# Optimization experiments

Hardware: AMD Instinct MI355X
Metric: run time of the kernel (lower is better)

The kernel has to match this reference:

```python
import jax, jax.numpy as jnp
import numpy as np

N_HEAD = 25

def setup_inputs() -> dict:
    key = jax.random.key(0)
    k1, k2, k3 = jax.random.split(key, 3)
    B, T, C = 2, 2048, 1600
    x = jax.random.normal(k1, (B, T, C), dtype=jnp.float32)
    w_qkv = jax.random.normal(k2, (C, 3 * C), dtype=jnp.float32) * (1.0 / np.sqrt(C))
    b_qkv = jnp.zeros((3 * C,), dtype=jnp.float32)
    w_out = jax.random.normal(k3, (C, C), dtype=jnp.float32) * (1.0 / np.sqrt(C))
    b_out = jnp.zeros((C,), dtype=jnp.float32)
    return {"x": x, "w_qkv": w_qkv, "b_qkv": b_qkv, "w_out": w_out, "b_out": b_out}

def reference(x, w_qkv, b_qkv, w_out, b_out):
    B, T, C = x.shape
    H = N_HEAD
    D = C // H  # head_dim = 64
    qkv = jnp.einsum('btc,cd->btd', x, w_qkv) + b_qkv  # [B,T,3C]
    q, k, v = jnp.split(qkv, 3, axis=-1)
    # [B,T,C] -> [B,H,T,D]
    q = q.reshape(B, T, H, D).transpose(0, 2, 1, 3)
    k = k.reshape(B, T, H, D).transpose(0, 2, 1, 3)
    v = v.reshape(B, T, H, D).transpose(0, 2, 1, 3)
    scale = 1.0 / jnp.sqrt(jnp.float32(D))
    scores = jnp.einsum('bhqd,bhkd->bhqk', q, k) * scale  # [B,H,T,T]
    causal = jnp.tril(jnp.ones((T, T), dtype=bool))
    scores = jnp.where(causal, scores, jnp.float32(-1e10))
    attn = jax.nn.softmax(scores, axis=-1)
    out = jnp.einsum('bhqk,bhkd->bhqd', attn, v)  # [B,H,T,D]
    out = out.transpose(0, 2, 1, 3).reshape(B, T, C)
    return jnp.einsum('btc,cd->btd', out, w_out) + b_out
```

## Files before the change

kernel.cpp:

```cpp
#include <hip/hip_runtime.h>
#include <cstdint>
#include <cstddef>

typedef unsigned short u16;
typedef __attribute__((ext_vector_type(8))) short bhalf8;
typedef __attribute__((ext_vector_type(4))) float fx4;
typedef __attribute__((ext_vector_type(4))) unsigned short u16x4;

#define T_SEQ 2048
#define NHEAD 25
#define QKV_LD 4864

static __device__ __forceinline__ u16 f2bf(float f) {
  union { float f; uint32_t u; } v; v.f = f;
  uint32_t r = (v.u + 0x7FFFu + ((v.u >> 16) & 1u)) >> 16;
  return (u16)r;
}

static __device__ __forceinline__ fx4 mfma16(bhalf8 a, bhalf8 b, fx4 c) {
  return __builtin_amdgcn_mfma_f32_16x16x32_bf16(a, b, c, 0, 0, 0);
}

static __device__ __forceinline__ void async16(const void* g, void* l) {
  __builtin_amdgcn_global_load_lds(
      (__attribute__((address_space(1))) unsigned int*)(void*)g,
      (__attribute__((address_space(3))) unsigned int*)l, 16, 0, 0);
}

__global__ void cvt_bf16_kernel(const float* __restrict__ in, u16* __restrict__ out, int n4) {
  int i = blockIdx.x * 256 + threadIdx.x;
  if (i >= n4) return;
  float4 v = ((const float4*)in)[i];
  u16x4 o;
  o.x = f2bf(v.x); o.y = f2bf(v.y); o.z = f2bf(v.z); o.w = f2bf(v.w);
  ((u16x4*)out)[i] = o;
}

__global__ void transp_cvt_kernel(const float* __restrict__ in, u16* __restrict__ out,
                                  int R, int C) {
  __shared__ float tile[32][33];
  int bx = blockIdx.x * 32, by = blockIdx.y * 32;
  int tx = threadIdx.x, ty = threadIdx.y;
  #pragma unroll
  for (int i = 0; i < 32; i += 8)
    tile[ty + i][tx] = in[(size_t)(by + ty + i) * C + bx + tx];
  __syncthreads();
  #pragma unroll
  for (int i = 0; i < 32; i += 8)
    out[(size_t)(bx + ty + i) * R + by + tx] = f2bf(tile[tx][ty + i]);
}

template<int BN, bool OUTF32>
__global__ __launch_bounds__(256)
void gemm_bt_kernel(const u16* __restrict__ A, const u16* __restrict__ BT,
                    const float* __restrict__ bias, void* __restrict__ C,
                    int K, int ldc, int Nreal) {
  constexpr int BM = 128, BK = 32;
  constexpr int NF = BN / 32;
  constexpr int APASS = (BM * BK) / (256 * 8);
  constexpr int BPASS = (BN * BK) / (256 * 8);
  __shared__ __align__(16) u16 Al[BM * BK];
  __shared__ __align__(16) u16 Bl[BN * BK];
  const int t = threadIdx.x;
  const int w = t >> 6, l = t & 63, lr = l & 15, lg = l >> 4;
  const int wm = w >> 1, wn = w & 1;

  const int nwg = gridDim.x * gridDim.y;
  const int id = blockIdx.y * gridDim.x + blockIdx.x;
  const int qq = nwg >> 3;
  const int swz = (id & 7) * qq + (id >> 3);
  const int bx = swz % gridDim.x, by = swz / gridDim.x;

  const int m0 = by * BM, n0 = bx * BN;

  fx4 acc[4][NF] = {};

  for (int k0 = 0; k0 < K; k0 += BK) {
    #pragma unroll
    for (int p = 0; p < APASS; ++p) {
      int c = t + p * 256;
      async16(A + (size_t)(m0 + (c >> 2)) * K + k0 + (c & 3) * 8, Al + c * 8);
    }
    #pragma unroll
    for (int p = 0; p < BPASS; ++p) {
      int c = t + p * 256;
      async16(BT + (size_t)(n0 + (c >> 2)) * K + k0 + (c & 3) * 8, Bl + c * 8);
    }
    __syncthreads();
    bhalf8 af[4], bfr[NF];
    #pragma unroll
    for (int m = 0; m < 4; ++m)
      af[m] = *(const bhalf8*)(Al + (wm * 64 + m * 16 + lr) * BK + lg * 8);
    #pragma unroll
    for (int n = 0; n < NF; ++n)
      bfr[n] = *(const bhalf8*)(Bl + (wn * (BN / 2) + n * 16 + lr) * BK + lg * 8);
    #pragma unroll
    for (int m = 0; m < 4; ++m)
      #pragma unroll
      for (int n = 0; n < NF; ++n)
        acc[m][n] = mfma16(af[m], bfr[n], acc[m][n]);
    __syncthreads();
  }

  #pragma unroll
  for (int m = 0; m < 4; ++m)
  #pragma unroll
  for (int n = 0; n < NF; ++n)
  #pragma unroll
  for (int r = 0; r < 4; ++r) {
    int gr = m0 + wm * 64 + m * 16 + lg * 4 + r;
    int gc = n0 + wn * (BN / 2) + n * 16 + lr;
    float bv = (gc < Nreal) ? bias[gc] : 0.0f;
    float v = acc[m][n][r] + bv;
    if constexpr (OUTF32) ((float*)C)[(size_t)gr * ldc + gc] = v;
    else                  ((u16*)C)[(size_t)gr * ldc + gc] = f2bf(v);
  }
}

#define KSWZ(row, slot) (((row) << 6) + ((((slot)) ^ ((row) & 7)) << 3))

__global__ __launch_bounds__(512, 4)
void attn_kernel(const u16* __restrict__ qkv, u16* __restrict__ out) {
  const int qblk = (gridDim.x - 1) - blockIdx.x;
  const int bh = blockIdx.y;
  const int b = bh / NHEAD, h = bh % NHEAD;
  const int t = threadIdx.x, w = t >> 6, l = t & 63;
  const int lr = l & 15, lg = l >> 4;

  __shared__ __align__(16) u16 Kl[2][64 * 64];
  __shared__ __align__(16) u16 Vt[2][64 * 64];
  __shared__ __align__(16) u16 Pl[8][16][72];

  const int q0 = qblk * 128;
  const int qw = q0 + w * 16;
  const int nkb = 2 * qblk + 2;

  const size_t qoff = ((size_t)(b * T_SEQ + qw + lr)) * QKV_LD + h * 64;
  bhalf8 qf0 = *(const bhalf8*)(qkv + qoff + lg * 8);
  bhalf8 qf1 = *(const bhalf8*)(qkv + qoff + 32 + lg * 8);

  constexpr float KSC = 0.125f * 1.44269504089f;

  fx4 oacc[4] = {};
  float m_run[4], mk[4], thr[4], l_acc[4];
  #pragma unroll
  for (int r = 0; r < 4; ++r) {
    m_run[r] = -3.0e38f; mk[r] = -3.0e38f; thr[r] = -3.0e38f; l_acc[r] = 0.0f;
  }

  const int krow = t >> 3;
  const int kslot = (t & 7) ^ (krow & 7);
  const int vrow = t >> 3;
  const int vcol = (t & 7) * 8;
  const size_t kvrow_base = (size_t)(b * T_SEQ) * QKV_LD + 1600 + h * 64;

  int4 vpre;
  {
    const size_t ks = kvrow_base + (size_t)krow * QKV_LD + kslot * 8;
    async16(qkv + ks, Kl[0] + t * 8);
    vpre = *(const int4*)(qkv + kvrow_base + (size_t)vrow * QKV_LD + 1600 + vcol);
  }

  for (int kb = 0; kb < nkb; ++kb) {
    const int bsel = kb & 1;
    const int kv0 = kb * 64;
    u16* Klb = Kl[bsel];
    u16* Vtb = Vt[bsel];

    asm volatile("s_waitcnt vmcnt(0)" ::: "memory");
    {
      union { int4 v; u16 u[8]; } vv; vv.v = vpre;
      #pragma unroll
      for (int i = 0; i < 8; ++i) {
        int row = vcol + i;
        Vtb[(row << 6) + (((vrow >> 3) ^ (row & 7)) << 3) + (vrow & 7)] = vv.u[i];
      }
    }
    __syncthreads();

    if (kb + 1 < nkb) {
      const size_t rb = kvrow_base + (size_t)(kv0 + 64 + krow) * QKV_LD;
      async16(qkv + rb + kslot * 8, Kl[bsel ^ 1] + t * 8);
      vpre = *(const int4*)(qkv + kvrow_base + (size_t)(kv0 + 64 + vrow) * QKV_LD + 1600 + vcol);
    }

    const bool active = (kv0 <= qw + 15);
    if (active) {
      float sv[4][4];
      #pragma unroll
      for (int n = 0; n < 4; ++n) {
        bhalf8 k0f = *(const bhalf8*)(Klb + KSWZ(n * 16 + lr, lg));
        bhalf8 k1f = *(const bhalf8*)(Klb + KSWZ(n * 16 + lr, 4 + lg));
        fx4 s = {0.f, 0.f, 0.f, 0.f};
        s = mfma16(qf0, k0f, s);
        s = mfma16(qf1, k1f, s);
        #pragma unroll
        for (int r = 0; r < 4; ++r) sv[n][r] = s[r];
      }
      if (kv0 + 63 > qw) {
        #pragma unroll
        for (int n = 0; n < 4; ++n)
          #pragma unroll
          for (int r = 0; r < 4; ++r)
            if (kv0 + n * 16 + lr > qw + lg * 4 + r) sv[n][r] = -1e30f;
      }
      float pm[4];
      bool ok = true;
      #pragma unroll
      for (int r = 0; r < 4; ++r) {
        pm[r] = fmaxf(fmaxf(sv[0][r], sv[1][r]), fmaxf(sv[2][r], sv[3][r]));
        ok = ok && (pm[r] <= thr[r]);
      }
      if (!__all(ok)) {
        #pragma unroll
        for (int r = 0; r < 4; ++r) {
          float mx = pm[r] * 0.125f;
          mx = fmaxf(mx, __shfl_xor(mx, 1));
          mx = fmaxf(mx, __shfl_xor(mx, 2));
          mx = fmaxf(mx, __shfl_xor(mx, 4));
          mx = fmaxf(mx, __shfl_xor(mx, 8));
          float mN = fmaxf(m_run[r], mx);
          float scl = __expf(m_run[r] - mN);
          m_run[r] = mN;
          mk[r] = mN * 1.44269504089f;
          thr[r] = 8.0f * mN + 64.0f;
          l_acc[r] *= scl;
          oacc[0][r] *= scl; oacc[1][r] *= scl; oacc[2][r] *= scl; oacc[3][r] *= scl;
        }
      }
      #pragma unroll
      for (int n = 0; n < 4; ++n)
        #pragma unroll
        for (int r = 0; r < 4; ++r) {
          float p = exp2f(fmaf(sv[n][r], KSC, -mk[r]));
          l_acc[r] += p;
          Pl[w][lg * 4 + r][n * 16 + lr] = f2bf(p);
        }
      asm volatile("s_waitcnt lgkmcnt(0)" ::: "memory");
      __builtin_amdgcn_sched_barrier(0);
      #pragma unroll
      for (int s = 0; s < 2; ++s) {
        bhalf8 pa = *(const bhalf8*)&Pl[w][lr][s * 32 + lg * 8];
        #pragma unroll
        for (int n = 0; n < 4; ++n) {
          bhalf8 vbf = *(const bhalf8*)(Vtb + KSWZ(n * 16 + lr, s * 4 + lg));
          oacc[n] = mfma16(pa, vbf, oacc[n]);
        }
      }
    }
  }

  #pragma unroll
  for (int r = 0; r < 4; ++r) {
    float rs = l_acc[r];
    rs += __shfl_xor(rs, 1);
    rs += __shfl_xor(rs, 2);
    rs += __shfl_xor(rs, 4);
    rs += __shfl_xor(rs, 8);
    l_acc[r] = rs;
  }
  const size_t obase = ((size_t)(b * T_SEQ + qw + lg * 4)) * 1600 + h * 64;
  #pragma unroll
  for (int n = 0; n < 4; ++n)
    #pragma unroll
    for (int r = 0; r < 4; ++r) {
      float v = oacc[n][r] / l_acc[r];
      out[obase + (size_t)r * 1600 + n * 16 + lr] = f2bf(v);
    }
}

extern "C" void kernel_launch(void* const* d_in, const int* in_sizes, int n_in,
                              void* d_out, int out_size, void* d_ws, size_t ws_size,
                              hipStream_t stream) {
  const float* x     = (const float*)d_in[0];
  const float* w_qkv = (const float*)d_in[1];
  const float* b_qkv = (const float*)d_in[2];
  const float* w_out = (const float*)d_in[3];
  const float* b_out = (const float*)d_in[4];
  float* out = (float*)d_out;

  constexpr size_t NTOK = 4096;
  char* ws = (char*)d_ws;
  size_t off = 0;
  u16* xb    = (u16*)(ws + off); off += NTOK * 1600 * 2;
  u16* wqkvT = (u16*)(ws + off); off += (size_t)QKV_LD * 1600 * 2;
  u16* woutT = (u16*)(ws + off); off += (size_t)1600 * 1600 * 2;
  u16* qkvb  = (u16*)(ws + off); off += NTOK * QKV_LD * 2;
  u16* attnb = (u16*)(ws + off); off += NTOK * 1600 * 2;
  (void)ws_size; (void)in_sizes; (void)n_in; (void)out_size;

  cvt_bf16_kernel<<<dim3((unsigned)(NTOK * 1600 / 4 / 256)), dim3(256), 0, stream>>>(
      x, xb, (int)(NTOK * 1600 / 4));
  transp_cvt_kernel<<<dim3(4800 / 32, 1600 / 32), dim3(32, 8), 0, stream>>>(
      w_qkv, wqkvT, 1600, 4800);
  transp_cvt_kernel<<<dim3(1600 / 32, 1600 / 32), dim3(32, 8), 0, stream>>>(
      w_out, woutT, 1600, 1600);
  gemm_bt_kernel<128, false><<<dim3(QKV_LD / 128, NTOK / 128), dim3(256), 0, stream>>>(
      xb, wqkvT, b_qkv, qkvb, 1600, QKV_LD, 4800);
  attn_kernel<<<dim3(T_SEQ / 128, 2 * NHEAD), dim3(512), 0, stream>>>(qkvb, attnb);
  gemm_bt_kernel<64, true><<<dim3(1600 / 64, NTOK / 128), dim3(256), 0, stream>>>(
      attnb, woutT, b_out, out, 1600, 1600, 1600);
}
```

Baseline: 437.4 us.

## Give each attention wave two query tiles and widen output GEMM tile

The attention kernel drops to 4 waves per block, and each wave now handles 32 query rows as two 16-row groups. Each K/V fragment read from LDS is reused across two MFMAs, which halves LDS traffic per unit of compute, at the cost of more registers and less occupancy. MFMA sections are wrapped in s_setprio. The output projection switches to a 128-wide N tile with a padded weight buffer (1664 columns) and a column guard on the store. The padded weight rows beyond 1600 are never written by the transpose, so they hold whatever was in the workspace, but their results are masked out.

```diff
diff --git a/kernel.cpp b/kernel.cpp
--- a/kernel.cpp
+++ b/kernel.cpp
@@ -10,6 +10,7 @@
 #define T_SEQ 2048
 #define NHEAD 25
 #define QKV_LD 4864
+#define WOUT_LD 1664
 
 static __device__ __forceinline__ u16 f2bf(float f) {
   union { float f; uint32_t u; } v; v.f = f;
@@ -112,14 +113,17 @@
     int gc = n0 + wn * (BN / 2) + n * 16 + lr;
     float bv = (gc < Nreal) ? bias[gc] : 0.0f;
     float v = acc[m][n][r] + bv;
-    if constexpr (OUTF32) ((float*)C)[(size_t)gr * ldc + gc] = v;
-    else                  ((u16*)C)[(size_t)gr * ldc + gc] = f2bf(v);
+    if constexpr (OUTF32) {
+      if (gc < Nreal) ((float*)C)[(size_t)gr * ldc + gc] = v;
+    } else {
+      ((u16*)C)[(size_t)gr * ldc + gc] = f2bf(v);
+    }
   }
 }
 
 #define KSWZ(row, slot) (((row) << 6) + ((((slot)) ^ ((row) & 7)) << 3))
 
-__global__ __launch_bounds__(512, 4)
+__global__ __launch_bounds__(256, 3)
 void attn_kernel(const u16* __restrict__ qkv, u16* __restrict__ out) {
   const int qblk = (gridDim.x - 1) - blockIdx.x;
   const int bh = blockIdx.y;
@@ -129,36 +133,42 @@
 
   __shared__ __align__(16) u16 Kl[2][64 * 64];
   __shared__ __align__(16) u16 Vt[2][64 * 64];
-  __shared__ __align__(16) u16 Pl[8][16][72];
+  __shared__ __align__(16) u16 Pl[4][32][72];
 
   const int q0 = qblk * 128;
-  const int qw = q0 + w * 16;
+  const int qw = q0 + w * 32;
   const int nkb = 2 * qblk + 2;
 
-  const size_t qoff = ((size_t)(b * T_SEQ + qw + lr)) * QKV_LD + h * 64;
-  bhalf8 qf0 = *(const bhalf8*)(qkv + qoff + lg * 8);
-  bhalf8 qf1 = *(const bhalf8*)(qkv + qoff + 32 + lg * 8);
+  bhalf8 qf[2][2];
+  #pragma unroll
+  for (int g = 0; g < 2; ++g) {
+    const size_t qoff = ((size_t)(b * T_SEQ + qw + g * 16 + lr)) * QKV_LD + h * 64;
+    qf[g][0] = *(const bhalf8*)(qkv + qoff + lg * 8);
+    qf[g][1] = *(const bhalf8*)(qkv + qoff + 32 + lg * 8);
+  }
 
   constexpr float KSC = 0.125f * 1.44269504089f;
 
-  fx4 oacc[4] = {};
-  float m_run[4], mk[4], thr[4], l_acc[4];
-  #pragma unroll
-  for (int r = 0; r < 4; ++r) {
-    m_run[r] = -3.0e38f; mk[r] = -3.0e38f; thr[r] = -3.0e38f; l_acc[r] = 0.0f;
-  }
-
-  const int krow = t >> 3;
-  const int kslot = (t & 7) ^ (krow & 7);
-  const int vrow = t >> 3;
-  const int vcol = (t & 7) * 8;
+  fx4 oacc[2][4] = {};
+  float m_run[2][4], mk[2][4], thr[2][4], l_acc[2][4];
+  #pragma unroll
+  for (int g = 0; g < 2; ++g)
+    #pragma unroll
+    for (int r = 0; r < 4; ++r) {
+      m_run[g][r] = -3.0e38f; mk[g][r] = -3.0e38f; thr[g][r] = -3.0e38f; l_acc[g][r] = 0.0f;
+    }
+
   const size_t kvrow_base = (size_t)(b * T_SEQ) * QKV_LD + 1600 + h * 64;
 
-  int4 vpre;
-  {
-    const size_t ks = kvrow_base + (size_t)krow * QKV_LD + kslot * 8;
-    async16(qkv + ks, Kl[0] + t * 8);
-    vpre = *(const int4*)(qkv + kvrow_base + (size_t)vrow * QKV_LD + 1600 + vcol);
+  int4 vpre[2];
+  #pragma unroll
+  for (int p = 0; p < 2; ++p) {
+    const int c = t + p * 256;
+    const int kr = c >> 3;
+    const int ks = (c & 7) ^ (kr & 7);
+    const size_t rb = kvrow_base + (size_t)kr * QKV_LD;
+    async16(qkv + rb + ks * 8, Kl[0] + c * 8);
+    vpre[p] = *(const int4*)(qkv + rb + 1600 + (c & 7) * 8);
   }
 
   for (int kb = 0; kb < nkb; ++kb) {
@@ -168,105 +178,136 @@
     u16* Vtb = Vt[bsel];
 
     asm volatile("s_waitcnt vmcnt(0)" ::: "memory");
-    {
-      union { int4 v; u16 u[8]; } vv; vv.v = vpre;
+    #pragma unroll
+    for (int p = 0; p < 2; ++p) {
+      const int c = t + p * 256;
+      const int vr = c >> 3;
+      const int vc = (c & 7) * 8;
+      union { int4 v; u16 u[8]; } vv; vv.v = vpre[p];
       #pragma unroll
       for (int i = 0; i < 8; ++i) {
-        int row = vcol + i;
-        Vtb[(row << 6) + (((vrow >> 3) ^ (row & 7)) << 3) + (vrow & 7)] = vv.u[i];
+        int row = vc + i;
+        Vtb[(row << 6) + (((vr >> 3) ^ (row & 7)) << 3) + (vr & 7)] = vv.u[i];
       }
     }
     __syncthreads();
 
     if (kb + 1 < nkb) {
-      const size_t rb = kvrow_base + (size_t)(kv0 + 64 + krow) * QKV_LD;
-      async16(qkv + rb + kslot * 8, Kl[bsel ^ 1] + t * 8);
-      vpre = *(const int4*)(qkv + kvrow_base + (size_t)(kv0 + 64 + vrow) * QKV_LD + 1600 + vcol);
-    }
-
-    const bool active = (kv0 <= qw + 15);
+      #pragma unroll
+      for (int p = 0; p < 2; ++p) {
+        const int c = t + p * 256;
+        const int kr = c >> 3;
+        const int ks = (c & 7) ^ (kr & 7);
+        const size_t rb = kvrow_base + (size_t)(kv0 + 64 + kr) * QKV_LD;
+        async16(qkv + rb + ks * 8, Kl[bsel ^ 1] + c * 8);
+        vpre[p] = *(const int4*)(qkv + rb + 1600 + (c & 7) * 8);
+      }
+    }
+
+    const bool active = (kv0 <= qw + 31);
     if (active) {
-      float sv[4][4];
+      float sv[2][4][4];
+      __builtin_amdgcn_s_setprio(1);
       #pragma unroll
       for (int n = 0; n < 4; ++n) {
         bhalf8 k0f = *(const bhalf8*)(Klb + KSWZ(n * 16 + lr, lg));
         bhalf8 k1f = *(const bhalf8*)(Klb + KSWZ(n * 16 + lr, 4 + lg));
-        fx4 s = {0.f, 0.f, 0.f, 0.f};
-        s = mfma16(qf0, k0f, s);
-        s = mfma16(qf1, k1f, s);
-        #pragma unroll
-        for (int r = 0; r < 4; ++r) sv[n][r] = s[r];
-      }
+        #pragma unroll
+        for (int g = 0; g < 2; ++g) {
+          fx4 s = {0.f, 0.f, 0.f, 0.f};
+          s = mfma16(qf[g][0], k0f, s);
+          s = mfma16(qf[g][1], k1f, s);
+          #pragma unroll
+          for (int r = 0; r < 4; ++r) sv[g][n][r] = s[r];
+        }
+      }
+      __builtin_amdgcn_s_setprio(0);
       if (kv0 + 63 > qw) {
+        #pragma unroll
+        for (int g = 0; g < 2; ++g)
+          #pragma unroll
+          for (int n = 0; n < 4; ++n)
+            #pragma unroll
+            for (int r = 0; r < 4; ++r)
+              if (kv0 + n * 16 + lr > qw + g * 16 + lg * 4 + r) sv[g][n][r] = -1e30f;
+      }
+      float pm[2][4];
+      bool ok = true;
+      #pragma unroll
+      for (int g = 0; g < 2; ++g)
+        #pragma unroll
+        for (int r = 0; r < 4; ++r) {
+          pm[g][r] = fmaxf(fmaxf(sv[g][0][r], sv[g][1][r]), fmaxf(sv[g][2][r], sv[g][3][r]));
+          ok = ok && (pm[g][r] <= thr[g][r]);
+        }
+      if (!__all(ok)) {
+        #pragma unroll
+        for (int g = 0; g < 2; ++g)
+          #pragma unroll
+          for (int r = 0; r < 4; ++r) {
+            float mx = pm[g][r] * 0.125f;
+            mx = fmaxf(mx, __shfl_xor(mx, 1));
+            mx = fmaxf(mx, __shfl_xor(mx, 2));
+            mx = fmaxf(mx, __shfl_xor(mx, 4));
+            mx = fmaxf(mx, __shfl_xor(mx, 8));
+            float mN = fmaxf(m_run[g][r], mx);
+            float scl = __expf(m_run[g][r] - mN);
+            m_run[g][r] = mN;
+            mk[g][r] = mN * 1.44269504089f;
+            thr[g][r] = 8.0f * mN + 64.0f;
+            l_acc[g][r] *= scl;
+            oacc[g][0][r] *= scl; oacc[g][1][r] *= scl;
+            oacc[g][2][r] *= scl; oacc[g][3][r] *= scl;
+          }
+      }
+      #pragma unroll
+      for (int g = 0; g < 2; ++g)
         #pragma unroll
         for (int n = 0; n < 4; ++n)
           #pragma unroll
-          for (int r = 0; r < 4; ++r)
-            if (kv0 + n * 16 + lr > qw + lg * 4 + r) sv[n][r] = -1e30f;
-      }
-      float pm[4];
-      bool ok = true;
-      #pragma unroll
-      for (int r = 0; r < 4; ++r) {
-        pm[r] = fmaxf(fmaxf(sv[0][r], sv[1][r]), fmaxf(sv[2][r], sv[3][r]));
-        ok = ok && (pm[r] <= thr[r]);
-      }
-      if (!__all(ok)) {
-        #pragma unroll
-        for (int r = 0; r < 4; ++r) {
-          float mx = pm[r] * 0.125f;
-          mx = fmaxf(mx, __shfl_xor(mx, 1));
-          mx = fmaxf(mx, __shfl_xor(mx, 2));
-          mx = fmaxf(mx, __shfl_xor(mx, 4));
-          mx = fmaxf(mx, __shfl_xor(mx, 8));
-          float mN = fmaxf(m_run[r], mx);
-          float scl = __expf(m_run[r] - mN);
-          m_run[r] = mN;
-          mk[r] = mN * 1.44269504089f;
-          thr[r] = 8.0f * mN + 64.0f;
-          l_acc[r] *= scl;
-          oacc[0][r] *= scl; oacc[1][r] *= scl; oacc[2][r] *= scl; oacc[3][r] *= scl;
-        }
-      }
-      #pragma unroll
-      for (int n = 0; n < 4; ++n)
-        #pragma unroll
-        for (int r = 0; r < 4; ++r) {
-          float p = exp2f(fmaf(sv[n][r], KSC, -mk[r]));
-          l_acc[r] += p;
-          Pl[w][lg * 4 + r][n * 16 + lr] = f2bf(p);
-        }
+          for (int r = 0; r < 4; ++r) {
+            float p = exp2f(fmaf(sv[g][n][r], KSC, -mk[g][r]));
+            l_acc[g][r] += p;
+            Pl[w][g * 16 + lg * 4 + r][n * 16 + lr] = f2bf(p);
+          }
       asm volatile("s_waitcnt lgkmcnt(0)" ::: "memory");
       __builtin_amdgcn_sched_barrier(0);
+      __builtin_amdgcn_s_setprio(1);
       #pragma unroll
       for (int s = 0; s < 2; ++s) {
-        bhalf8 pa = *(const bhalf8*)&Pl[w][lr][s * 32 + lg * 8];
+        bhalf8 pa0 = *(const bhalf8*)&Pl[w][lr][s * 32 + lg * 8];
+        bhalf8 pa1 = *(const bhalf8*)&Pl[w][16 + lr][s * 32 + lg * 8];
         #pragma unroll
         for (int n = 0; n < 4; ++n) {
           bhalf8 vbf = *(const bhalf8*)(Vtb + KSWZ(n * 16 + lr, s * 4 + lg));
-          oacc[n] = mfma16(pa, vbf, oacc[n]);
+          oacc[0][n] = mfma16(pa0, vbf, oacc[0][n]);
+          oacc[1][n] = mfma16(pa1, vbf, oacc[1][n]);
         }
       }
-    }
-  }
-
-  #pragma unroll
-  for (int r = 0; r < 4; ++r) {
-    float rs = l_acc[r];
-    rs += __shfl_xor(rs, 1);
-    rs += __shfl_xor(rs, 2);
-    rs += __shfl_xor(rs, 4);
-    rs += __shfl_xor(rs, 8);
-    l_acc[r] = rs;
-  }
-  const size_t obase = ((size_t)(b * T_SEQ + qw + lg * 4)) * 1600 + h * 64;
-  #pragma unroll
-  for (int n = 0; n < 4; ++n)
+      __builtin_amdgcn_s_setprio(0);
+    }
+  }
+
+  #pragma unroll
+  for (int g = 0; g < 2; ++g) {
     #pragma unroll
     for (int r = 0; r < 4; ++r) {
-      float v = oacc[n][r] / l_acc[r];
-      out[obase + (size_t)r * 1600 + n * 16 + lr] = f2bf(v);
-    }
+      float rs = l_acc[g][r];
+      rs += __shfl_xor(rs, 1);
+      rs += __shfl_xor(rs, 2);
+      rs += __shfl_xor(rs, 4);
+      rs += __shfl_xor(rs, 8);
+      l_acc[g][r] = rs;
+    }
+    const size_t obase = ((size_t)(b * T_SEQ + qw + g * 16 + lg * 4)) * 1600 + h * 64;
+    #pragma unroll
+    for (int n = 0; n < 4; ++n)
+      #pragma unroll
+      for (int r = 0; r < 4; ++r) {
+        float v = oacc[g][n][r] / l_acc[g][r];
+        out[obase + (size_t)r * 1600 + n * 16 + lr] = f2bf(v);
+      }
+  }
 }
 
 extern "C" void kernel_launch(void* const* d_in, const int* in_sizes, int n_in,
@@ -284,7 +325,7 @@
   size_t off = 0;
   u16* xb    = (u16*)(ws + off); off += NTOK * 1600 * 2;
   u16* wqkvT = (u16*)(ws + off); off += (size_t)QKV_LD * 1600 * 2;
-  u16* woutT = (u16*)(ws + off); off += (size_t)1600 * 1600 * 2;
+  u16* woutT = (u16*)(ws + off); off += (size_t)WOUT_LD * 1600 * 2;
   u16* qkvb  = (u16*)(ws + off); off += NTOK * QKV_LD * 2;
   u16* attnb = (u16*)(ws + off); off += NTOK * 1600 * 2;
   (void)ws_size; (void)in_sizes; (void)n_in; (void)out_size;
@@ -297,7 +338,7 @@
       w_out, woutT, 1600, 1600);
   gemm_bt_kernel<128, false><<<dim3(QKV_LD / 128, NTOK / 128), dim3(256), 0, stream>>>(
       xb, wqkvT, b_qkv, qkvb, 1600, QKV_LD, 4800);
-  attn_kernel<<<dim3(T_SEQ / 128, 2 * NHEAD), dim3(512), 0, stream>>>(qkvb, attnb);
-  gemm_bt_kernel<64, true><<<dim3(1600 / 64, NTOK / 128), dim3(256), 0, stream>>>(
+  attn_kernel<<<dim3(T_SEQ / 128, 2 * NHEAD), dim3(256), 0, stream>>>(qkvb, attnb);
+  gemm_bt_kernel<128, true><<<dim3(WOUT_LD / 128, NTOK / 128), dim3(256), 0, stream>>>(
       attnb, woutT, b_out, out, 1600, 1600, 1600);
 }
```

After: 446.4 us. 2.1% more time.
